# Performance work log

Hardware: AMD Instinct MI355X
Metric: run time of the kernel (lower is better)

The kernel has to match this reference:

```python
import jax, jax.numpy as jnp
import numpy as np

INV_SQRT3 = 1.0 / np.sqrt(3.0)


def setup_inputs() -> dict:
    key = jax.random.key(0)
    ks = jax.random.split(key, 7)
    N = 100000
    M0, M1 = 128, 64  # multiplicities of 0e and 1o irreps in in1 / out
    data_in1 = jax.random.normal(ks[0], (N, M0 + 3 * M1), jnp.float32)  # [N, 320]
    data_in2 = jax.random.normal(ks[1], (N, 1 + 3), jnp.float32)        # [N, 4] = 1x0e + 1x1o
    # e3nn-style path weights, standard normal init (path_normalization='none')
    W00 = jax.random.normal(ks[2], (M0, 1, M0), jnp.float32)  # 0e x 0e -> 0e
    W01 = jax.random.normal(ks[3], (M0, 1, M1), jnp.float32)  # 0e x 1o -> 1o
    W10 = jax.random.normal(ks[4], (M1, 1, M1), jnp.float32)  # 1o x 0e -> 1o
    W11 = jax.random.normal(ks[5], (M1, 1, M0), jnp.float32)  # 1o x 1o -> 0e
    # fan_in of the scalar output slice = 128*1 (0e x 0e) + 64*1 (1o x 1o) = 192
    sqrt_k = 1.0 / np.sqrt(M0 + M1)
    bias = jax.random.uniform(ks[6], (M0,), jnp.float32, -sqrt_k, sqrt_k)
    return {"data_in1": data_in1, "data_in2": data_in2,
            "W00": W00, "W01": W01, "W10": W10, "W11": W11, "bias": bias}


def reference(data_in1, data_in2, W00, W01, W10, W11, bias):
    M0, M1 = W00.shape[0], W10.shape[0]
    N = data_in1.shape[0]
    s1 = data_in1[:, :M0]                      # [N, 128]  scalars 0e
    v1 = data_in1[:, M0:].reshape(N, M1, 3)    # [N, 64, 3] vectors 1o
    s2 = data_in2[:, :1]                       # [N, 1]    scalar attr
    v2 = data_in2[:, 1:].reshape(N, 1, 3)      # [N, 1, 3] vector attr
    # CG paths (component irrep-normalization, path_normalization='none'):
    # wigner-3j folded analytically; net per-path coefs are 1,1,1,1/sqrt(3)
    out0 = jnp.einsum('nu,nv,uvw->nw', s1, s2, W00)                       # 0e x 0e -> 0e
    out0 = out0 + INV_SQRT3 * jnp.einsum('nui,nvi,uvw->nw', v1, v2, W11)  # 1o x 1o -> 0e
    outv = jnp.einsum('nu,nvk,uvw->nwk', s1, v2, W01)                     # 0e x 1o -> 1o
    outv = outv + jnp.einsum('nuk,nv,uvw->nwk', v1, s2, W10)              # 1o x 0e -> 1o
    # indexed bias add: bias_idx selects the l=0 output slice [0:M0]
    out0 = out0 + bias
    return jnp.concatenate([out0, outv.reshape(N, M1 * 3)], axis=1)      # [N, 320]
```

## Files before the change

kernel.cpp:

```cpp
#include <hip/hip_runtime.h>

typedef __bf16 bf16_8 __attribute__((ext_vector_type(8)));
typedef float  f32x4  __attribute__((ext_vector_type(4)));
typedef float  f32x3  __attribute__((ext_vector_type(3), aligned(4)));

#define INV_SQRT3f 0.57735026918962576f


__global__ void tp_convert_weights(
    const float* __restrict__ W00, const float* __restrict__ W01,
    const float* __restrict__ W10, const float* __restrict__ W11,
    __bf16* __restrict__ ws)
{
    const int chunk = blockIdx.x * blockDim.x + threadIdx.x;
    bf16_8 v;
    if (chunk < 2048) {
        const int c = chunk >> 4, q = chunk & 15;
#pragma unroll
        for (int j = 0; j < 8; ++j) v[j] = (__bf16)W00[(q * 8 + j) * 128 + c];
        *(bf16_8*)(ws + (c * 16 + (q ^ (c & 15))) * 8) = v;
    } else if (chunk < 3072) {
        const int idx = chunk - 2048;
        const int c = idx >> 4, q = idx & 15;
#pragma unroll
        for (int j = 0; j < 8; ++j) v[j] = (__bf16)W01[(q * 8 + j) * 64 + c];
        *(bf16_8*)(ws + 16384 + idx * 8) = v;
    } else if (chunk < 4096) {
        const int idx = chunk - 3072;
        const int c = idx >> 3, q = idx & 7;
#pragma unroll
        for (int j = 0; j < 8; ++j) v[j] = (__bf16)W11[(q * 8 + j) * 128 + c];
        *(bf16_8*)(ws + 24576 + idx * 8) = v;
    } else if (chunk < 4608) {
        const int idx = chunk - 4096;
        const int c = idx >> 3, q = idx & 7;
#pragma unroll
        for (int j = 0; j < 8; ++j) v[j] = (__bf16)W10[(q * 8 + j) * 64 + c];
        *(bf16_8*)(ws + 32768 + idx * 8) = v;
    }
}

#define LOAD_S1(P1, D2, S) do {                                               \
    int _row = (S) * 16 + mh;  if (_row >= N) _row = N - 1;                   \
    const float* _r1 = din1 + _row * 320 + 8 * kq;                            \
    _Pragma("unroll")                                                         \
    for (int _t = 0; _t < 4; ++_t) {                                          \
        P1[2 * _t]     = *(const f32x4*)(_r1 + 32 * _t);                      \
        P1[2 * _t + 1] = *(const f32x4*)(_r1 + 32 * _t + 4);                  \
    }                                                                         \
    D2 = *(const f32x4*)(din2 + _row * 4);                                    \
} while (0)

#define LOAD_S2(P2, S) do {                                                   \
    int _row = (S) * 16 + mh;  if (_row >= N) _row = N - 1;                   \
    const float* _r2 = din1 + _row * 320 + 128 + 24 * kq;                     \
    _Pragma("unroll")                                                         \
    for (int _h = 0; _h < 2; ++_h)                                            \
        _Pragma("unroll")                                                     \
        for (int _q = 0; _q < 6; ++_q)                                        \
            P2[6 * _h + _q] = *(const f32x4*)(_r2 + 96 * _h + 4 * _q);        \
} while (0)

#define PH1(P1, D2) do {                                                      \
    _Pragma("unroll")                                                         \
    for (int _i = 0; _i < 8; ++_i) accA[_i] = (f32x4)0.0f;                    \
    _Pragma("unroll")                                                         \
    for (int _k = 0; _k < 3; ++_k)                                            \
        _Pragma("unroll")                                                     \
        for (int _i = 0; _i < 4; ++_i) accV[_k][_i] = (f32x4)0.0f;            \
    _Pragma("unroll")                                                         \
    for (int _s = 0; _s < 4; ++_s) {                                          \
        const f32x4 _x0 = P1[2 * _s];                                         \
        const f32x4 _x1 = P1[2 * _s + 1];                                     \
        float _xx[8] = {_x0.x, _x0.y, _x0.z, _x0.w, _x1.x, _x1.y, _x1.z, _x1.w}; \
        bf16_8 _as2, _av0, _av1, _av2;                                        \
        _Pragma("unroll")                                                     \
        for (int _j = 0; _j < 8; ++_j) {                                      \
            _as2[_j] = (__bf16)(D2.x * _xx[_j]);                              \
            _av0[_j] = (__bf16)(D2.y * _xx[_j]);                              \
            _av1[_j] = (__bf16)(D2.z * _xx[_j]);                              \
            _av2[_j] = (__bf16)(D2.w * _xx[_j]);                              \
        }                                                                     \
        const int _q = 4 * _s + kq;                                           \
        _Pragma("unroll")                                                     \
        for (int _nt = 0; _nt < 8; ++_nt) {                                   \
            const int _c = _nt * 16 + mh;                                     \
            bf16_8 _b = *(const bf16_8*)(sw00 + (_c * 16 + (_q ^ mh)) * 8);   \
            accA[_nt] = __builtin_amdgcn_mfma_f32_16x16x32_bf16(_as2, _b, accA[_nt], 0, 0, 0); \
        }                                                                     \
        _Pragma("unroll")                                                     \
        for (int _nt = 0; _nt < 4; ++_nt) {                                   \
            const int _c = _nt * 16 + mh;                                     \
            bf16_8 _b = *(const bf16_8*)(w01g + (_c * 16 + _q) * 8);          \
            accV[0][_nt] = __builtin_amdgcn_mfma_f32_16x16x32_bf16(_av0, _b, accV[0][_nt], 0, 0, 0); \
            accV[1][_nt] = __builtin_amdgcn_mfma_f32_16x16x32_bf16(_av1, _b, accV[1][_nt], 0, 0, 0); \
            accV[2][_nt] = __builtin_amdgcn_mfma_f32_16x16x32_bf16(_av2, _b, accV[2][_nt], 0, 0, 0); \
        }                                                                     \
    }                                                                         \
} while (0)

#define PH2(P2, D2) do {                                                      \
    _Pragma("unroll")                                                         \
    for (int _s = 0; _s < 2; ++_s) {                                          \
        float _b24[24];                                                       \
        _Pragma("unroll")                                                     \
        for (int _qq = 0; _qq < 6; ++_qq) {                                   \
            const f32x4 _t4 = P2[6 * _s + _qq];                               \
            _b24[4 * _qq]     = _t4.x; _b24[4 * _qq + 1] = _t4.y;             \
            _b24[4 * _qq + 2] = _t4.z; _b24[4 * _qq + 3] = _t4.w;             \
        }                                                                     \
        bf16_8 _at, _ac0, _ac1, _ac2;                                         \
        _Pragma("unroll")                                                     \
        for (int _j = 0; _j < 8; ++_j) {                                      \
            const float _e0 = _b24[3 * _j], _e1 = _b24[3 * _j + 1], _e2 = _b24[3 * _j + 2]; \
            _at[_j]  = (__bf16)(INV_SQRT3f * (_e0 * D2.y + _e1 * D2.z + _e2 * D2.w)); \
            _ac0[_j] = (__bf16)(D2.x * _e0);                                  \
            _ac1[_j] = (__bf16)(D2.x * _e1);                                  \
            _ac2[_j] = (__bf16)(D2.x * _e2);                                  \
        }                                                                     \
        const int _q = 4 * _s + kq;                                           \
        _Pragma("unroll")                                                     \
        for (int _nt = 0; _nt < 8; ++_nt) {                                   \
            const int _c = _nt * 16 + mh;                                     \
            bf16_8 _b = *(const bf16_8*)(w11g + (_c * 8 + _q) * 8);           \
            accA[_nt] = __builtin_amdgcn_mfma_f32_16x16x32_bf16(_at, _b, accA[_nt], 0, 0, 0); \
        }                                                                     \
        _Pragma("unroll")                                                     \
        for (int _nt = 0; _nt < 4; ++_nt) {                                   \
            const int _c = _nt * 16 + mh;                                     \
            bf16_8 _b = *(const bf16_8*)(w10g + (_c * 8 + _q) * 8);           \
            accV[0][_nt] = __builtin_amdgcn_mfma_f32_16x16x32_bf16(_ac0, _b, accV[0][_nt], 0, 0, 0); \
            accV[1][_nt] = __builtin_amdgcn_mfma_f32_16x16x32_bf16(_ac1, _b, accV[1][_nt], 0, 0, 0); \
            accV[2][_nt] = __builtin_amdgcn_mfma_f32_16x16x32_bf16(_ac2, _b, accV[2][_nt], 0, 0, 0); \
        }                                                                     \
    }                                                                         \
} while (0)

#define EPI(S) do {                                                           \
    const int _r0 = (S) * 16;                                                 \
    if (_r0 + 16 <= N) {                                                      \
        _Pragma("unroll")                                                     \
        for (int _p = 0; _p < 2; ++_p) {                                      \
            asm volatile("s_waitcnt lgkmcnt(0)" ::: "memory");                \
            if ((kq >> 1) == _p) {                                            \
                const int _rl = 4 * (kq & 1);                                 \
                _Pragma("unroll")                                             \
                for (int _nt = 0; _nt < 8; ++_nt) {                           \
                    const float _bi = bias[_nt * 16 + mh];                    \
                    _Pragma("unroll")                                         \
                    for (int _r = 0; _r < 4; ++_r) {                          \
                        const int _rw = _rl + _r;                             \
                        const int _ch = (_nt * 4 + (mh >> 2)) ^ _rw;          \
                        stgw[_rw * 320 + _ch * 4 + (mh & 3)] = accA[_nt][_r] + _bi; \
                    }                                                         \
                }                                                             \
                _Pragma("unroll")                                             \
                for (int _nt = 0; _nt < 4; ++_nt) {                           \
                    _Pragma("unroll")                                         \
                    for (int _r = 0; _r < 4; ++_r) {                          \
                        const int _rw = _rl + _r;                             \
                        _Pragma("unroll")                                     \
                        for (int _k = 0; _k < 3; ++_k) {                      \
                            const int _f = 128 + 3 * (_nt * 16 + mh) + _k;    \
                            const int _ch = (_f >> 2) ^ _rw;                  \
                            stgw[_rw * 320 + _ch * 4 + (_f & 3)] = accV[_k][_nt][_r]; \
                        }                                                     \
                    }                                                         \
                }                                                             \
            }                                                                 \
            asm volatile("s_waitcnt lgkmcnt(0)" ::: "memory");                \
            __builtin_amdgcn_sched_barrier(0);                                \
            float* _gbase = out + (_r0 + _p * 8) * 320;                       \
            _Pragma("unroll")                                                 \
            for (int _i = 0; _i < 10; ++_i) {                                 \
                const int _v  = _i * 64 + lane;                               \
                const int _rw = _v / 80;                                      \
                const int _ch = (_v % 80) ^ _rw;                              \
                f32x4 _d = *(const f32x4*)(stgw + _rw * 320 + _ch * 4);       \
                __builtin_nontemporal_store(_d, (f32x4*)(_gbase + _v * 4));   \
            }                                                                 \
        }                                                                     \
    } else {                                                                  \
        const int _rowg0 = _r0 + 4 * kq;                                      \
        _Pragma("unroll")                                                     \
        for (int _nt = 0; _nt < 8; ++_nt) {                                   \
            const float _bi = bias[_nt * 16 + mh];                            \
            _Pragma("unroll")                                                 \
            for (int _r = 0; _r < 4; ++_r) {                                  \
                const int _rowg = _rowg0 + _r;                                \
                if (_rowg < N)                                                \
                    __builtin_nontemporal_store(accA[_nt][_r] + _bi,          \
                                                out + _rowg * 320 + _nt * 16 + mh); \
            }                                                                 \
        }                                                                     \
        _Pragma("unroll")                                                     \
        for (int _r = 0; _r < 4; ++_r) {                                      \
            const int _rowg = _rowg0 + _r;                                    \
            if (_rowg < N) {                                                  \
                _Pragma("unroll")                                             \
                for (int _nt = 0; _nt < 4; ++_nt) {                           \
                    const int _w = _nt * 16 + mh;                             \
                    f32x3 _o;                                                 \
                    _o.x = accV[0][_nt][_r];                                  \
                    _o.y = accV[1][_nt][_r];                                  \
                    _o.z = accV[2][_nt][_r];                                  \
                    __builtin_nontemporal_store(_o,                           \
                        (f32x3*)(out + _rowg * 320 + 128 + 3 * _w));          \
                }                                                             \
            }                                                                 \
        }                                                                     \
    }                                                                         \
} while (0)

__global__ __launch_bounds__(256, 2) void tp_main_kernel(
    const float* __restrict__ din1, const float* __restrict__ din2,
    const __bf16* __restrict__ wsw, const float* __restrict__ bias,
    float* __restrict__ out, int N, int npairs)
{
    __shared__ __attribute__((aligned(16))) __bf16 smem[36864];
    const __bf16* sw00 = smem;
    float* stgbase = (float*)(smem + 16384);

    const int tid  = threadIdx.x;
    const int wid  = (blockIdx.x << 2) + (tid >> 6);
    const int lane = tid & 63;
    const int mh   = lane & 15;
    const int kq   = lane >> 4;
    float* stgw = stgbase + (tid >> 6) * 2560;

    const __bf16* __restrict__ w01g = wsw + 16384;
    const __bf16* __restrict__ w11g = wsw + 24576;
    const __bf16* __restrict__ w10g = wsw + 32768;

    const int spair = wid < npairs ? wid : npairs - 1;
    const int sA = 2 * spair, sB = 2 * spair + 1;

    f32x4 fill[8];
    {
        const f32x4* s = (const f32x4*)wsw;
#pragma unroll
        for (int i = 0; i < 8; ++i) fill[i] = s[tid + 256 * i];
    }

    f32x4 p1A[8], p2A[12], d2A;
    f32x4 p1B[8], p2B[12], d2B;
    LOAD_S1(p1A, d2A, sA);
    LOAD_S2(p2A, sA);

    {
        f32x4* d = (f32x4*)smem;
#pragma unroll
        for (int i = 0; i < 8; ++i) d[tid + 256 * i] = fill[i];
    }
    __syncthreads();

    if (wid < npairs) {
        f32x4 accA[8];
        f32x4 accV[3][4];

        PH1(p1A, d2A);
        LOAD_S1(p1B, d2B, sB);
        PH2(p2A, d2A);
        LOAD_S2(p2B, sB);
        EPI(sA);

        PH1(p1B, d2B);
        PH2(p2B, d2B);
        EPI(sB);
    }
}

extern "C" void kernel_launch(void* const* d_in, const int* in_sizes, int n_in,
                              void* d_out, int out_size, void* d_ws, size_t ws_size,
                              hipStream_t stream)
{
    const float* din1 = (const float*)d_in[0];
    const float* din2 = (const float*)d_in[1];
    const float* W00  = (const float*)d_in[2];
    const float* W01  = (const float*)d_in[3];
    const float* W10  = (const float*)d_in[4];
    const float* W11  = (const float*)d_in[5];
    const float* bias = (const float*)d_in[6];
    float* outp = (float*)d_out;
    __bf16* ws = (__bf16*)d_ws;

    const int N = in_sizes[0] / 320;
    const int npairs  = (N + 31) / 32;
    const int nblocks = (npairs + 3) / 4;

    hipLaunchKernelGGL(tp_convert_weights, dim3(18), dim3(256), 0, stream,
                       W00, W01, W10, W11, ws);
    hipLaunchKernelGGL(tp_main_kernel, dim3(nblocks), dim3(256), 0, stream,
                       din1, din2, ws, bias, outp, N, npairs);
}
```

Baseline: 288.6 us.

## Shrink staging LDS and reuse prefetch registers to fit three blocks per CU

The epilogue staging buffer is halved by writing four rows per pass instead of eight, so each wave stages in four passes. The A and B prefetch register arrays are merged into one set, and the bias values are hoisted into registers once per wave. Together with launch bounds raised to three blocks, this is meant to cut LDS and VGPR use so more waves run per CU. In exchange the epilogue needs more barrier passes, and reusing the prefetch registers may create a dependency that limits overlap between loads and MFMA work.

```diff
diff --git a/kernel.cpp b/kernel.cpp
--- a/kernel.cpp
+++ b/kernel.cpp
@@ -140,39 +140,35 @@
     const int _r0 = (S) * 16;                                                 \
     if (_r0 + 16 <= N) {                                                      \
         _Pragma("unroll")                                                     \
-        for (int _p = 0; _p < 2; ++_p) {                                      \
+        for (int _p = 0; _p < 4; ++_p) {                                      \
             asm volatile("s_waitcnt lgkmcnt(0)" ::: "memory");                \
-            if ((kq >> 1) == _p) {                                            \
-                const int _rl = 4 * (kq & 1);                                 \
+            if (kq == _p) {                                                   \
                 _Pragma("unroll")                                             \
                 for (int _nt = 0; _nt < 8; ++_nt) {                           \
-                    const float _bi = bias[_nt * 16 + mh];                    \
                     _Pragma("unroll")                                         \
                     for (int _r = 0; _r < 4; ++_r) {                          \
-                        const int _rw = _rl + _r;                             \
-                        const int _ch = (_nt * 4 + (mh >> 2)) ^ _rw;          \
-                        stgw[_rw * 320 + _ch * 4 + (mh & 3)] = accA[_nt][_r] + _bi; \
+                        const int _ch = (_nt * 4 + (mh >> 2)) ^ _r;           \
+                        stgw[_r * 320 + _ch * 4 + (mh & 3)] = accA[_nt][_r] + biasr[_nt]; \
                     }                                                         \
                 }                                                             \
                 _Pragma("unroll")                                             \
                 for (int _nt = 0; _nt < 4; ++_nt) {                           \
                     _Pragma("unroll")                                         \
                     for (int _r = 0; _r < 4; ++_r) {                          \
-                        const int _rw = _rl + _r;                             \
                         _Pragma("unroll")                                     \
                         for (int _k = 0; _k < 3; ++_k) {                      \
                             const int _f = 128 + 3 * (_nt * 16 + mh) + _k;    \
-                            const int _ch = (_f >> 2) ^ _rw;                  \
-                            stgw[_rw * 320 + _ch * 4 + (_f & 3)] = accV[_k][_nt][_r]; \
+                            const int _ch = (_f >> 2) ^ _r;                   \
+                            stgw[_r * 320 + _ch * 4 + (_f & 3)] = accV[_k][_nt][_r]; \
                         }                                                     \
                     }                                                         \
                 }                                                             \
             }                                                                 \
             asm volatile("s_waitcnt lgkmcnt(0)" ::: "memory");                \
             __builtin_amdgcn_sched_barrier(0);                                \
-            float* _gbase = out + (_r0 + _p * 8) * 320;                       \
+            float* _gbase = out + (_r0 + _p * 4) * 320;                       \
             _Pragma("unroll")                                                 \
-            for (int _i = 0; _i < 10; ++_i) {                                 \
+            for (int _i = 0; _i < 5; ++_i) {                                  \
                 const int _v  = _i * 64 + lane;                               \
                 const int _rw = _v / 80;                                      \
                 const int _ch = (_v % 80) ^ _rw;                              \
@@ -184,12 +180,11 @@
         const int _rowg0 = _r0 + 4 * kq;                                      \
         _Pragma("unroll")                                                     \
         for (int _nt = 0; _nt < 8; ++_nt) {                                   \
-            const float _bi = bias[_nt * 16 + mh];                            \
             _Pragma("unroll")                                                 \
             for (int _r = 0; _r < 4; ++_r) {                                  \
                 const int _rowg = _rowg0 + _r;                                \
                 if (_rowg < N)                                                \
-                    __builtin_nontemporal_store(accA[_nt][_r] + _bi,          \
+                    __builtin_nontemporal_store(accA[_nt][_r] + biasr[_nt],   \
                                                 out + _rowg * 320 + _nt * 16 + mh); \
             }                                                                 \
         }                                                                     \
@@ -212,12 +207,12 @@
     }                                                                         \
 } while (0)
 
-__global__ __launch_bounds__(256, 2) void tp_main_kernel(
+__global__ __launch_bounds__(256, 3) void tp_main_kernel(
     const float* __restrict__ din1, const float* __restrict__ din2,
     const __bf16* __restrict__ wsw, const float* __restrict__ bias,
     float* __restrict__ out, int N, int npairs)
 {
-    __shared__ __attribute__((aligned(16))) __bf16 smem[36864];
+    __shared__ __attribute__((aligned(16))) __bf16 smem[26624];
     const __bf16* sw00 = smem;
     float* stgbase = (float*)(smem + 16384);
 
@@ -226,7 +221,7 @@
     const int lane = tid & 63;
     const int mh   = lane & 15;
     const int kq   = lane >> 4;
-    float* stgw = stgbase + (tid >> 6) * 2560;
+    float* stgw = stgbase + (tid >> 6) * 1280;
 
     const __bf16* __restrict__ w01g = wsw + 16384;
     const __bf16* __restrict__ w11g = wsw + 24576;
@@ -242,10 +237,9 @@
         for (int i = 0; i < 8; ++i) fill[i] = s[tid + 256 * i];
     }
 
-    f32x4 p1A[8], p2A[12], d2A;
-    f32x4 p1B[8], p2B[12], d2B;
-    LOAD_S1(p1A, d2A, sA);
-    LOAD_S2(p2A, sA);
+    f32x4 p1[8], p2[12], d2A, d2B;
+    LOAD_S1(p1, d2A, sA);
+    LOAD_S2(p2, sA);
 
     {
         f32x4* d = (f32x4*)smem;
@@ -255,17 +249,21 @@
     __syncthreads();
 
     if (wid < npairs) {
+        float biasr[8];
+#pragma unroll
+        for (int i = 0; i < 8; ++i) biasr[i] = bias[i * 16 + mh];
+
         f32x4 accA[8];
         f32x4 accV[3][4];
 
-        PH1(p1A, d2A);
-        LOAD_S1(p1B, d2B, sB);
-        PH2(p2A, d2A);
-        LOAD_S2(p2B, sB);
+        PH1(p1, d2A);
+        LOAD_S1(p1, d2B, sB);
+        PH2(p2, d2A);
+        LOAD_S2(p2, sB);
         EPI(sA);
 
-        PH1(p1B, d2B);
-        PH2(p2B, d2B);
+        PH1(p1, d2B);
+        PH2(p2, d2B);
         EPI(sB);
     }
 }
```

Measured after the change: 328.2 us. 1.14x slower.
